# Kernel optimization log

Hardware: AMD Instinct MI355X
Metric: run time of the kernel (lower is better)

Reference implementation:

```python
import jax, jax.numpy as jnp
import numpy as np

ANNEAL_T_START = 5.0
T_END = 1.0


def setup_inputs() -> dict:
    key = jax.random.key(0)
    ks = jax.random.split(key, 8)
    B, V, H, CD, WID = 8192, 1024, 128, 16, 64
    return {
        "cond": jax.random.normal(ks[0], (B, CD), jnp.float32),
        "W": 0.01 * jax.random.normal(ks[1], (V, H), jnp.float32),
        "b": 0.01 * jax.random.normal(ks[2], (V,), jnp.float32),
        "c": 0.01 * jax.random.normal(ks[3], (H,), jnp.float32),
        "fc1_w": jax.random.normal(ks[4], (WID, CD), jnp.float32) / np.float32(np.sqrt(CD)),
        "fc1_b": jnp.zeros((WID,), jnp.float32),
        "fc2_w": jax.random.normal(ks[5], (2 * (V + H), WID), jnp.float32) / np.float32(np.sqrt(WID)),
        "fc2_b": jnp.zeros((2 * (V + H),), jnp.float32),
        "falloff": jnp.float32(1.0),
        "steps": 16,
    }


def _bern(key, p):
    # Bernoulli sample as float of same dtype as p.
    return (jax.random.uniform(key, p.shape, p.dtype) < p).astype(p.dtype)


def reference(cond, W, b, c, fc1_w, fc1_b, fc2_w, fc2_b, falloff, steps):
    V, H = W.shape
    B = cond.shape[0]
    dtype = W.dtype

    # Conditioner: FiLM-style modulation of visible/hidden biases.
    x = jnp.tanh(cond @ fc1_w.T + fc1_b)
    x = x @ fc2_w.T + fc2_b  # [B, 2*(V+H)]
    gamma_b = x[:, :V]
    beta_b = x[:, V:2 * V]
    gamma_c = x[:, 2 * V:2 * V + H]
    beta_c = x[:, 2 * V + H:]
    b_mod = (1.0 + gamma_b) * b + beta_b  # [B, V]
    c_mod = (1.0 + gamma_c) * c + beta_c  # [B, H]
    bsum = jnp.sum(b_mod, axis=-1)  # [B], constant across steps

    # Annealing temperature schedule (sigmoid falloff).
    t = jnp.arange(steps, dtype=dtype)
    s = 1.0 / (1.0 + jnp.exp(falloff * (t - steps / 2.0)))
    temps = T_END + (ANNEAL_T_START - T_END) * s  # [steps]

    base = jax.random.key(42)
    v0 = _bern(jax.random.fold_in(base, 2 ** 20), jnp.full((B, V), 0.5, dtype))
    s0_0 = jnp.ones((B, 1), dtype)

    def flip(v, s0):
        return s0 * v + (1.0 - s0) * (1.0 - v)

    def step(carry, xs):
        v, s0 = carry
        i, T = xs
        k1, k2, k3 = jax.random.split(jax.random.fold_in(base, i), 3)
        v_eff = flip(v, s0)
        p_h = jax.nn.sigmoid((v_eff @ W + c_mod) / T)  # [B, H]
        h = _bern(k1, p_h)
        a = h @ W.T  # [B, V]
        vb = jnp.sum(v * b_mod, axis=-1)
        va = jnp.sum(v * a, axis=-1)
        dE = -bsum - jnp.sum(a, axis=-1) + 2.0 * vb + 2.0 * va  # [B]
        p_s0 = jax.nn.sigmoid(dE / T)
        s0n = _bern(k2, p_s0)[:, None]  # [B, 1]
        p_v = jax.nn.sigmoid((a + b_mod) / T)
        v_samp = _bern(k3, p_v)
        v_next = flip(v_samp, s0n)
        return (v_next, s0n), None

    (v, _), _ = jax.lax.scan(
        step, (v0, s0_0), (jnp.arange(steps, dtype=jnp.int32), temps)
    )
    return v
```

## Files before the change

kernel.cpp:

```cpp
#include <hip/hip_runtime.h>
#include <stdint.h>

#pragma clang fp contract(off)

#define B_ 8192
#define V_ 1024
#define H_ 128
#define CD_ 16
#define WID_ 64
#define NOUT_ 2304
#define STEPS_ 16

typedef float f32x2 __attribute__((ext_vector_type(2)));

__device__ __forceinline__ void pkfma(f32x2& acc, f32x2 wv, f32x2 bf2) {
  asm("v_pk_fma_f32 %0, %1, %2, %0" : "+v"(acc) : "v"(wv), "v"(bf2));
}

__host__ __device__ __forceinline__ void tf2x32(uint32_t k0, uint32_t k1,
                                                uint32_t x0, uint32_t x1,
                                                uint32_t* o0, uint32_t* o1) {
  uint32_t ks2 = k0 ^ k1 ^ 0x1BD11BDAu;
#define RL_(v, d) (((v) << (d)) | ((v) >> (32 - (d))))
#define RND_(a) { x0 += x1; x1 = RL_(x1, a); x1 ^= x0; }
  x0 += k0; x1 += k1;
  RND_(13) RND_(15) RND_(26) RND_(6)
  x0 += k1; x1 += ks2 + 1u;
  RND_(17) RND_(29) RND_(16) RND_(24)
  x0 += ks2; x1 += k0 + 2u;
  RND_(13) RND_(15) RND_(26) RND_(6)
  x0 += k0; x1 += k1 + 3u;
  RND_(17) RND_(29) RND_(16) RND_(24)
  x0 += k1; x1 += ks2 + 4u;
  RND_(13) RND_(15) RND_(26) RND_(6)
  x0 += ks2; x1 += k0 + 5u;
#undef RND_
#undef RL_
  *o0 = x0; *o1 = x1;
}

struct Keys { uint32_t a[6]; };

__device__ __forceinline__ uint32_t draw_bits(uint32_t ka, uint32_t kb, uint32_t j) {
  uint32_t x0, x1;
  tf2x32(ka, kb, 0u, j, &x0, &x1);
  return x0 ^ x1;
}

__device__ __forceinline__ float bits_to_u(uint32_t bits) {
  return __fsub_rn(__uint_as_float((bits >> 9) | 0x3f800000u), 1.0f);
}

__device__ __forceinline__ float exp_a(float x) {
  float xc = fminf(fmaxf(x, -88.3762626647949f), 88.3762626647950f);
  float fx = floorf(__fadd_rn(__fmul_rn(xc, 1.44269504088896341f), 0.5f));
  float xr = __fsub_rn(xc, __fmul_rn(0.693359375f, fx));
  xr = __fsub_rn(xr, __fmul_rn(-2.12194440e-4f, fx));
  float zz = __fmul_rn(xr, xr);
  float y = 1.9875691500E-4f;
  y = __fadd_rn(__fmul_rn(y, xr), 1.3981999507E-3f);
  y = __fadd_rn(__fmul_rn(y, xr), 8.3334519073E-3f);
  y = __fadd_rn(__fmul_rn(y, xr), 4.1665795894E-2f);
  y = __fadd_rn(__fmul_rn(y, xr), 1.6666665459E-1f);
  y = __fadd_rn(__fmul_rn(y, xr), 5.0000001201E-1f);
  y = __fadd_rn(__fmul_rn(y, zz), xr);
  y = __fadd_rn(y, 1.0f);
  int n = (int)fx;
  float sc = __int_as_float((n + 127) << 23);
  return __fmul_rn(y, sc);
}

__device__ __forceinline__ float tanh_a(float xin) {
  float x = fmaxf(fminf(xin, 7.90531110763549805f), -7.90531110763549805f);
  float x2 = __fmul_rn(x, x);
  float p = __fadd_rn(__fmul_rn(x2, -2.76076847742355e-16f), 2.00018790482477e-13f);
  p = __fadd_rn(__fmul_rn(x2, p), -8.60467152213735e-11f);
  p = __fadd_rn(__fmul_rn(x2, p), 5.12229709037114e-08f);
  p = __fadd_rn(__fmul_rn(x2, p), 1.48572235717979e-05f);
  p = __fadd_rn(__fmul_rn(x2, p), 6.37261928875436e-04f);
  p = __fadd_rn(__fmul_rn(x2, p), 4.89352455891786e-03f);
  p = __fmul_rn(x, p);
  float q = __fadd_rn(__fmul_rn(x2, 1.19825839466702e-06f), 1.18534705686654e-04f);
  q = __fadd_rn(__fmul_rn(x2, q), 2.26843463243900e-03f);
  q = __fadd_rn(__fmul_rn(x2, q), 4.89352518554385e-03f);
  float r = p / q;
  if (fabsf(xin) < 0.0004f) r = xin;
  return r;
}

__device__ __forceinline__ float sigmoid_a(float z) {
  float e = exp_a(-z);
  return 1.0f / __fadd_rn(1.0f, e);
}

__global__ void k_transpose(const float* __restrict__ W, float* __restrict__ WT,
                            const float* __restrict__ fc2w, float* __restrict__ fc2T) {
  int i = blockIdx.x * blockDim.x + threadIdx.x;
  if (i < V_ * H_) { int v = i / H_, h = i % H_; WT[h * V_ + v] = W[i]; }
  if (i < NOUT_ * WID_) { int j = i / WID_, w = i % WID_; fc2T[w * NOUT_ + j] = fc2w[i]; }
}

__global__ void k_temps(const float* __restrict__ falloff, float* __restrict__ temps) {
  int t = threadIdx.x;
  if (t < 16) {
    float arg = __fmul_rn(*falloff, __fsub_rn((float)t, 8.0f));
    float e = exp_a(arg);
    float s = 1.0f / __fadd_rn(1.0f, e);
    temps[t] = __fadd_rn(1.0f, __fmul_rn(4.0f, s));
  }
}

__global__ void k_mlp1(const float* __restrict__ cond, const float* __restrict__ fc1w,
                       const float* __restrict__ fc1b, float* __restrict__ xout) {
  int idx = blockIdx.x * blockDim.x + threadIdx.x;
  if (idx >= B_ * WID_) return;
  int row = idx >> 6, w = idx & 63;
  float acc = 0.0f;
  for (int k = 0; k < CD_; k++) acc = __fmaf_rn(cond[row * CD_ + k], fc1w[w * CD_ + k], acc);
  float z = __fadd_rn(acc, fc1b[w]);
  xout[idx] = tanh_a(z);
}

__global__ __launch_bounds__(128) void k_mlp2b(const float* __restrict__ xmlp,
                       const float* __restrict__ fc2T, const float* __restrict__ fc2b,
                       const float* __restrict__ bvec, float* __restrict__ b_mod) {
  __shared__ float xs[32][WID_];
  int jbase = blockIdx.x * 128;
  int r0 = blockIdx.y * 32;
  int tid = threadIdx.x;
  for (int t = tid; t < 32 * WID_; t += 128)
    xs[t >> 6][t & 63] = xmlp[(r0 + (t >> 6)) * WID_ + (t & 63)];
  __syncthreads();
  int j = jbase + tid;
  float accg[32], accb[32];
#pragma unroll
  for (int r = 0; r < 32; r++) { accg[r] = 0.0f; accb[r] = 0.0f; }
  for (int w = 0; w < WID_; w++) {
    float fg = fc2T[w * NOUT_ + j];
    float fb = fc2T[w * NOUT_ + 1024 + j];
#pragma unroll
    for (int r = 0; r < 32; r++) {
      float xv = xs[r][w];
      accg[r] = __fmaf_rn(xv, fg, accg[r]);
      accb[r] = __fmaf_rn(xv, fb, accb[r]);
    }
  }
  float bj = bvec[j];
  float biasg = fc2b[j], biasb = fc2b[1024 + j];
#pragma unroll
  for (int r = 0; r < 32; r++) {
    float g = __fadd_rn(accg[r], biasg);
    float bb = __fadd_rn(accb[r], biasb);
    float t1 = __fadd_rn(1.0f, g);
    b_mod[(r0 + r) * V_ + j] = __fadd_rn(__fmul_rn(t1, bj), bb);
  }
}

__global__ __launch_bounds__(128) void k_mlp2c(const float* __restrict__ xmlp,
                       const float* __restrict__ fc2T, const float* __restrict__ fc2b,
                       const float* __restrict__ cvec, float* __restrict__ c_mod) {
  __shared__ float xs[32][WID_];
  int r0 = blockIdx.y * 32;
  int tid = threadIdx.x;
  for (int t = tid; t < 32 * WID_; t += 128)
    xs[t >> 6][t & 63] = xmlp[(r0 + (t >> 6)) * WID_ + (t & 63)];
  __syncthreads();
  float accg[32], accb[32];
#pragma unroll
  for (int r = 0; r < 32; r++) { accg[r] = 0.0f; accb[r] = 0.0f; }
  for (int w = 0; w < WID_; w++) {
    float fg = fc2T[w * NOUT_ + 2048 + tid];
    float fb = fc2T[w * NOUT_ + 2176 + tid];
#pragma unroll
    for (int r = 0; r < 32; r++) {
      float xv = xs[r][w];
      accg[r] = __fmaf_rn(xv, fg, accg[r]);
      accb[r] = __fmaf_rn(xv, fb, accb[r]);
    }
  }
  float cj = cvec[tid];
  float biasg = fc2b[2048 + tid], biasb = fc2b[2176 + tid];
#pragma unroll
  for (int r = 0; r < 32; r++) {
    float g = __fadd_rn(accg[r], biasg);
    float bb = __fadd_rn(accb[r], biasb);
    float t1 = __fadd_rn(1.0f, g);
    c_mod[(r0 + r) * H_ + tid] = __fadd_rn(__fmul_rn(t1, cj), bb);
  }
}

__global__ __launch_bounds__(64) void k_bsum(const float* __restrict__ b_mod,
                                             float* __restrict__ bsum) {
  int row = blockIdx.x * 64 + threadIdx.x;
  const float4* bp = (const float4*)(b_mod + (size_t)row * V_);
  float acc = 0.0f;
  for (int c = 0; c < 32; c++) {
    float4 Bv[8];
#pragma unroll
    for (int q = 0; q < 8; q++) Bv[q] = bp[c * 8 + q];
#pragma unroll
    for (int q = 0; q < 8; q++) {
      acc = __fadd_rn(acc, Bv[q].x);
      acc = __fadd_rn(acc, Bv[q].y);
      acc = __fadd_rn(acc, Bv[q].z);
      acc = __fadd_rn(acc, Bv[q].w);
    }
  }
  bsum[row] = acc;
}

__global__ void k_v0(uint32_t* __restrict__ v_bits, float* __restrict__ s0,
                     uint32_t kva, uint32_t kvb) {
  int idx = blockIdx.x * blockDim.x + threadIdx.x;
  int row = idx >> 10, col = idx & 1023;
  uint32_t bits = draw_bits(kva, kvb, (uint32_t)idx);
  float u = bits_to_u(bits);
  unsigned long long m = __ballot(u < 0.5f);
  if ((threadIdx.x & 63) == 0) {
    v_bits[row * 32 + (col >> 5)] = (uint32_t)m;
    v_bits[row * 32 + (col >> 5) + 1] = (uint32_t)(m >> 32);
  }
  if (col == 0) s0[row] = 1.0f;
}

__global__ __launch_bounds__(256) void k_h(const float* __restrict__ W,
                   const float* __restrict__ c_mod, const uint32_t* __restrict__ v_bits,
                   uint32_t* __restrict__ h_bits, const float* __restrict__ temps,
                   int step, Keys kn) {
  __shared__ uint32_t nib[16][32];
  int tid = threadIdx.x;
  int ct = tid & 31;
  int rt = tid >> 5;
  int h0 = ct << 2;
  int row0 = blockIdx.x * 16 + rt * 2;
  float T = temps[step];
  f32x2 a00 = {0.f, 0.f}, a01 = {0.f, 0.f};
  f32x2 a10 = {0.f, 0.f}, a11 = {0.f, 0.f};
  const float* wp = W + h0;
  const uint4* vb0q = (const uint4*)(v_bits + (size_t)row0 * 32);
  const uint4* vb1q = (const uint4*)(v_bits + (size_t)(row0 + 1) * 32);

  float4 A[8], Bq[8];
  uint32_t m0, m1;
  auto LOADW = [&](float4* d, int kbase) {
#pragma unroll
    for (int i = 0; i < 8; i++)
      d[i] = *(const float4*)(wp + (size_t)(kbase + i) * H_);
  };
  auto DO8 = [&](const float4* wv) {
#pragma unroll
    for (int j = 0; j < 8; j++) {
      uint32_t s0m = (uint32_t)((int32_t)m0 >> 31); m0 <<= 1;
      uint32_t s1m = (uint32_t)((int32_t)m1 >> 31); m1 <<= 1;
      float bf0 = __uint_as_float(s0m & 0x3f800000u);
      float bf1 = __uint_as_float(s1m & 0x3f800000u);
      f32x2 wlo = {wv[j].x, wv[j].y};
      f32x2 whi = {wv[j].z, wv[j].w};
      f32x2 b0 = {bf0, bf0};
      f32x2 b1 = {bf1, bf1};
      pkfma(a00, wlo, b0); pkfma(a01, whi, b0);
      pkfma(a10, wlo, b1); pkfma(a11, whi, b1);
    }
  };

  uint4 q0 = vb0q[0], q1 = vb1q[0];
  uint4 q0n, q1n;
  LOADW(A, 0);
  for (int kq = 0; kq < 8; kq++) {
    if (kq < 7) { q0n = vb0q[kq + 1]; q1n = vb1q[kq + 1]; }
    const uint32_t w0s[4] = {q0.x, q0.y, q0.z, q0.w};
    const uint32_t w1s[4] = {q1.x, q1.y, q1.z, q1.w};
#pragma unroll
    for (int wq = 0; wq < 4; wq++) {
      int kb = kq * 128 + wq * 32;
      m0 = __brev(w0s[wq]);
      m1 = __brev(w1s[wq]);
      LOADW(Bq, kb + 8);  DO8(A);
      LOADW(A, kb + 16);  DO8(Bq);
      LOADW(Bq, kb + 24); DO8(A);
      if (kb + 32 < 1024) LOADW(A, kb + 32);
      DO8(Bq);
    }
    q0 = q0n; q1 = q1n;
  }

  const f32x2* accs[2][2] = {{&a00, &a01}, {&a10, &a11}};
#pragma unroll
  for (int r = 0; r < 2; r++) {
    int row = row0 + r;
    float4 cm = *(const float4*)(c_mod + (size_t)row * H_ + h0);
    const float cma[4] = {cm.x, cm.y, cm.z, cm.w};
    const float ac[4] = {(*accs[r][0])[0], (*accs[r][0])[1],
                         (*accs[r][1])[0], (*accs[r][1])[1]};
    uint32_t nb = 0;
#pragma unroll
    for (int e = 0; e < 4; e++) {
      float z = __fadd_rn(ac[e], cma[e]) / T;
      float p = sigmoid_a(z);
      uint32_t b = draw_bits(kn.a[0], kn.a[1], (uint32_t)(row * H_ + h0 + e));
      if (bits_to_u(b) < p) nb |= 1u << e;
    }
    nib[rt * 2 + r][ct] = nb;
  }
  __syncthreads();
  if (tid < 64) {
    int rloc = tid >> 2, wq = tid & 3;
    uint32_t word = 0;
#pragma unroll
    for (int i = 0; i < 8; i++) word |= nib[rloc][wq * 8 + i] << (4 * i);
    h_bits[(size_t)(blockIdx.x * 16 + rloc) * 4 + wq] = word;
  }
}

__global__ __launch_bounds__(256) void k_a(const float* __restrict__ WT,
                   const uint32_t* __restrict__ h_bits, float* __restrict__ a) {
  int tid = threadIdx.x;
  int ct = tid & 63;
  int rt = tid >> 6;
  int v0 = blockIdx.x * 256 + (ct << 2);
  int r0 = blockIdx.y * 32 + rt * 8;
  f32x2 acc[8][2];
#pragma unroll
  for (int r = 0; r < 8; r++) { acc[r][0] = f32x2{0.f, 0.f}; acc[r][1] = f32x2{0.f, 0.f}; }
  uint4 hw[8];
#pragma unroll
  for (int r = 0; r < 8; r++) hw[r] = *(const uint4*)(h_bits + (size_t)(r0 + r) * 4);
  const float* wp0 = WT + v0;

  uint32_t m[8];
  float4 buf0[4], buf1[4];
  auto LOADG = [&](float4* d, int g) {
    const float* wp = wp0 + (size_t)(g * 4) * V_;
#pragma unroll
    for (int jj = 0; jj < 4; jj++) d[jj] = *(const float4*)(wp + (size_t)jj * V_);
  };
  auto COMP = [&](const float4* d) {
#pragma unroll
    for (int jj = 0; jj < 4; jj++) {
      f32x2 wlo = {d[jj].x, d[jj].y};
      f32x2 whi = {d[jj].z, d[jj].w};
#pragma unroll
      for (int r = 0; r < 8; r++) {
        uint32_t sm = (uint32_t)((int32_t)m[r] >> 31);
        m[r] <<= 1;
        float bf = __uint_as_float(sm & 0x3f800000u);
        f32x2 b2 = {bf, bf};
        pkfma(acc[r][0], wlo, b2);
        pkfma(acc[r][1], whi, b2);
      }
    }
  };

  LOADG(buf0, 0);
#pragma unroll
  for (int g = 0; g < 32; g++) {
    if ((g & 7) == 0) {
      const int s = g >> 3;
#pragma unroll
      for (int r = 0; r < 8; r++)
        m[r] = __brev(s == 0 ? hw[r].x : s == 1 ? hw[r].y : s == 2 ? hw[r].z : hw[r].w);
    }
    if (g & 1) { if (g < 31) LOADG(buf0, g + 1); COMP(buf1); }
    else       { if (g < 31) LOADG(buf1, g + 1); COMP(buf0); }
  }

#pragma unroll
  for (int r = 0; r < 8; r++) {
    float4 o = make_float4(acc[r][0][0], acc[r][0][1], acc[r][1][0], acc[r][1][1]);
    *(float4*)(a + (size_t)(r0 + r) * V_ + v0) = o;
  }
}

__global__ __launch_bounds__(256) void k_sv(const float* __restrict__ a,
                     const float* __restrict__ b_mod, const float* __restrict__ bsum,
                     const uint32_t* __restrict__ vb_old, uint32_t* __restrict__ vb_new,
                     float* __restrict__ s0, const float* __restrict__ temps,
                     int step, Keys kn) {
  __shared__ float As[2][16][132];
  __shared__ float Bs[2][16][132];
  int tid = threadIdx.x;
  int r0 = blockIdx.x * 16;
  float T = temps[step];
  int wv = tid >> 6;
  int lane = tid & 63;

  auto STAGE = [&](int buf, int c) {
#pragma unroll
    for (int i = 0; i < 2; i++) {
      int e = tid + i * 256;
      int r = e >> 5, c4 = e & 31;
      float4 av = *(const float4*)(a + (size_t)(r0 + r) * V_ + c * 128 + c4 * 4);
      float4 bv = *(const float4*)(b_mod + (size_t)(r0 + r) * V_ + c * 128 + c4 * 4);
      *(float4*)&As[buf][r][c4 * 4] = av;
      *(float4*)&Bs[buf][r][c4 * 4] = bv;
    }
  };

  float suma = 0.0f, vb = 0.0f, va = 0.0f;
  uint32_t flipm = 0;
  if (tid < 16) flipm = (s0[r0 + tid] == 0.0f) ? 0xFFFFFFFFu : 0u;
  STAGE(0, 0);
  __syncthreads();
  for (int c = 0; c < 8; c++) {
    if (c < 7) STAGE((c + 1) & 1, c + 1);
#pragma unroll
    for (int i = 0; i < 8; i++) {
      int e = tid + i * 256;
      int rl = e >> 7, cl = e & 127;
      float av = As[c & 1][rl][cl];
      float bv = Bs[c & 1][rl][cl];
      float z = __fadd_rn(av, bv) / T;
      float p = sigmoid_a(z);
      int row = r0 + rl;
      int col = c * 128 + cl;
      uint32_t bits = draw_bits(kn.a[4], kn.a[5], (uint32_t)(row * V_ + col));
      float u = bits_to_u(bits);
      unsigned long long mball = __ballot(u < p);
      if (lane == 0) {
        int base = row * 32 + (col >> 5);
        vb_new[base] = (uint32_t)mball;
        vb_new[base + 1] = (uint32_t)(mball >> 32);
      }
    }
    if (tid < 16) {
      int row = r0 + tid;
      uint4 mw = *(const uint4*)(vb_old + (size_t)row * 32 + c * 4);
      const uint32_t mm[4] = {mw.x ^ flipm, mw.y ^ flipm, mw.z ^ flipm, mw.w ^ flipm};
#pragma unroll
      for (int w4 = 0; w4 < 4; w4++) {
        uint32_t m = mm[w4];
#pragma unroll
        for (int j4 = 0; j4 < 8; j4++) {
          float4 av4 = *(const float4*)&As[c & 1][tid][w4 * 32 + j4 * 4];
          float4 bv4 = *(const float4*)&Bs[c & 1][tid][w4 * 32 + j4 * 4];
          const float ax[4] = {av4.x, av4.y, av4.z, av4.w};
          const float bx[4] = {bv4.x, bv4.y, bv4.z, bv4.w};
#pragma unroll
          for (int e = 0; e < 4; e++) {
            float bit = (float)((m >> (j4 * 4 + e)) & 1u);
            suma = __fadd_rn(suma, ax[e]);
            vb = __fmaf_rn(bx[e], bit, vb);
            va = __fmaf_rn(ax[e], bit, va);
          }
        }
      }
    }
    __syncthreads();
  }
  if (tid < 16) {
    int row = r0 + tid;
    float dE = __fsub_rn(-bsum[row], suma);
    dE = __fadd_rn(dE, __fmul_rn(2.0f, vb));
    dE = __fadd_rn(dE, __fmul_rn(2.0f, va));
    float p = sigmoid_a(dE / T);
    uint32_t bits = draw_bits(kn.a[2], kn.a[3], (uint32_t)row);
    float u = bits_to_u(bits);
    s0[row] = (u < p) ? 1.0f : 0.0f;
  }
}

__global__ void k_fin(const uint32_t* __restrict__ v_bits, const float* __restrict__ s0,
                      float* __restrict__ vout) {
  int idx = blockIdx.x * blockDim.x + threadIdx.x;
  int row = idx >> 10, col = idx & 1023;
  uint32_t w = v_bits[row * 32 + (col >> 5)];
  uint32_t bit = (w >> (col & 31)) & 1u;
  uint32_t eff = (s0[row] != 0.0f) ? bit : (bit ^ 1u);
  vout[idx] = (float)eff;
}

extern "C" void kernel_launch(void* const* d_in, const int* in_sizes, int n_in,
                              void* d_out, int out_size, void* d_ws, size_t ws_size,
                              hipStream_t stream) {
  const float* cond = (const float*)d_in[0];
  const float* W = (const float*)d_in[1];
  const float* bvec = (const float*)d_in[2];
  const float* cvec = (const float*)d_in[3];
  const float* fc1w = (const float*)d_in[4];
  const float* fc1b = (const float*)d_in[5];
  const float* fc2w = (const float*)d_in[6];
  const float* fc2b = (const float*)d_in[7];
  const float* falloff = (const float*)d_in[8];
  float* out = (float*)d_out;

  char* ws = (char*)d_ws;
  size_t off = 0;
  auto alloc = [&](size_t bytes) { void* p = ws + off; off += (bytes + 255) & ~(size_t)255; return p; };
  float* b_mod = (float*)alloc((size_t)B_ * V_ * 4);
  float* c_mod = (float*)alloc((size_t)B_ * H_ * 4);
  float* abuf  = (float*)alloc((size_t)B_ * V_ * 4);
  float* xmlp  = (float*)alloc((size_t)B_ * WID_ * 4);
  float* bsum  = (float*)alloc((size_t)B_ * 4);
  float* s0    = (float*)alloc((size_t)B_ * 4);
  uint32_t* v_bits0 = (uint32_t*)alloc((size_t)B_ * 32 * 4);
  uint32_t* v_bits1 = (uint32_t*)alloc((size_t)B_ * 32 * 4);
  uint32_t* h_bits = (uint32_t*)alloc((size_t)B_ * 4 * 4);
  float* WT    = (float*)alloc((size_t)H_ * V_ * 4);
  float* fc2T  = (float*)alloc((size_t)WID_ * NOUT_ * 4);
  float* temps = (float*)alloc(16 * 4);
  uint32_t* vb[2] = {v_bits0, v_bits1};

  uint32_t kva, kvb;
  tf2x32(0u, 42u, 0u, 1048576u, &kva, &kvb);
  Keys kn[16];
  for (int i = 0; i < 16; i++) {
    uint32_t f0, f1;
    tf2x32(0u, 42u, 0u, (uint32_t)i, &f0, &f1);
    uint32_t a0, a1;
    tf2x32(f0, f1, 0u, 0u, &a0, &a1); kn[i].a[0] = a0; kn[i].a[1] = a1;
    tf2x32(f0, f1, 0u, 1u, &a0, &a1); kn[i].a[2] = a0; kn[i].a[3] = a1;
    tf2x32(f0, f1, 0u, 2u, &a0, &a1); kn[i].a[4] = a0; kn[i].a[5] = a1;
  }

  k_transpose<<<(NOUT_ * WID_ + 255) / 256, 256, 0, stream>>>(W, WT, fc2w, fc2T);
  k_temps<<<1, 64, 0, stream>>>(falloff, temps);
  k_mlp1<<<(B_ * WID_) / 256, 256, 0, stream>>>(cond, fc1w, fc1b, xmlp);
  k_mlp2b<<<dim3(8, 256), 128, 0, stream>>>(xmlp, fc2T, fc2b, bvec, b_mod);
  k_mlp2c<<<dim3(1, 256), 128, 0, stream>>>(xmlp, fc2T, fc2b, cvec, c_mod);
  k_bsum<<<B_ / 64, 64, 0, stream>>>(b_mod, bsum);
  k_v0<<<(B_ * V_) / 256, 256, 0, stream>>>(vb[0], s0, kva, kvb);

  for (int i = 0; i < STEPS_; i++) {
    k_h<<<B_ / 16, 256, 0, stream>>>(W, c_mod, vb[i & 1], h_bits, temps, i, kn[i]);
    k_a<<<dim3(4, B_ / 32), 256, 0, stream>>>(WT, h_bits, abuf);
    k_sv<<<B_ / 16, 256, 0, stream>>>(abuf, b_mod, bsum, vb[i & 1], vb[(i + 1) & 1],
                                      s0, temps, i, kn[i]);
  }

  k_fin<<<(B_ * V_) / 256, 256, 0, stream>>>(vb[0], s0, out);
}
```

Before: 2.986 ms.

## Fuse visible-unit Bernoulli sampling into the h@W.T epilogue kernel

Visible sampling (sigmoid of a+b_mod, RNG draw, bit packing) moves out of the combined sample/energy kernel and into the epilogue of k_a, which packs its nibbles through shared memory into vb_new. The remaining k_s0 kernel only reduces the energy difference and samples s0. The sampling loop stays on full-block parallelism, now while the accumulators are still in registers, and k_s0 no longer does the per-element RNG work. In exchange, k_a does extra work, reads b_mod, and needs more shared memory and a block barrier.

```diff
diff --git a/kernel.cpp b/kernel.cpp
--- a/kernel.cpp
+++ b/kernel.cpp
@@ -313,7 +313,10 @@
 }
 
 __global__ __launch_bounds__(256) void k_a(const float* __restrict__ WT,
-                   const uint32_t* __restrict__ h_bits, float* __restrict__ a) {
+                   const uint32_t* __restrict__ h_bits, const float* __restrict__ b_mod,
+                   float* __restrict__ a, uint32_t* __restrict__ vb_new,
+                   const float* __restrict__ temps, int step, Keys kn) {
+  __shared__ uint32_t nib[32][65];
   int tid = threadIdx.x;
   int ct = tid & 63;
   int rt = tid >> 6;
@@ -364,25 +367,44 @@
     else       { if (g < 31) LOADG(buf1, g + 1); COMP(buf0); }
   }
 
+  float T = temps[step];
 #pragma unroll
   for (int r = 0; r < 8; r++) {
-    float4 o = make_float4(acc[r][0][0], acc[r][0][1], acc[r][1][0], acc[r][1][1]);
-    *(float4*)(a + (size_t)(r0 + r) * V_ + v0) = o;
-  }
-}
-
-__global__ __launch_bounds__(256) void k_sv(const float* __restrict__ a,
+    int row = r0 + r;
+    float4 av = make_float4(acc[r][0][0], acc[r][0][1], acc[r][1][0], acc[r][1][1]);
+    *(float4*)(a + (size_t)row * V_ + v0) = av;
+    float4 bv = *(const float4*)(b_mod + (size_t)row * V_ + v0);
+    const float ax[4] = {av.x, av.y, av.z, av.w};
+    const float bx[4] = {bv.x, bv.y, bv.z, bv.w};
+    uint32_t nb = 0;
+#pragma unroll
+    for (int e = 0; e < 4; e++) {
+      float z = __fadd_rn(ax[e], bx[e]) / T;
+      float p = sigmoid_a(z);
+      uint32_t bits = draw_bits(kn.a[4], kn.a[5], (uint32_t)(row * V_ + v0 + e));
+      float u = bits_to_u(bits);
+      if (u < p) nb |= 1u << e;
+    }
+    nib[rt * 8 + r][ct] = nb;
+  }
+  __syncthreads();
+  {
+    int rloc = tid >> 3, wq = tid & 7;
+    uint32_t word = 0;
+#pragma unroll
+    for (int i = 0; i < 8; i++) word |= nib[rloc][wq * 8 + i] << (4 * i);
+    vb_new[(size_t)(blockIdx.y * 32 + rloc) * 32 + blockIdx.x * 8 + wq] = word;
+  }
+}
+
+__global__ __launch_bounds__(256) void k_s0(const float* __restrict__ a,
                      const float* __restrict__ b_mod, const float* __restrict__ bsum,
-                     const uint32_t* __restrict__ vb_old, uint32_t* __restrict__ vb_new,
-                     float* __restrict__ s0, const float* __restrict__ temps,
-                     int step, Keys kn) {
+                     const uint32_t* __restrict__ vb_old, float* __restrict__ s0,
+                     const float* __restrict__ temps, int step, Keys kn) {
   __shared__ float As[2][16][132];
   __shared__ float Bs[2][16][132];
   int tid = threadIdx.x;
   int r0 = blockIdx.x * 16;
-  float T = temps[step];
-  int wv = tid >> 6;
-  int lane = tid & 63;
 
   auto STAGE = [&](int buf, int c) {
 #pragma unroll
@@ -403,25 +425,6 @@
   __syncthreads();
   for (int c = 0; c < 8; c++) {
     if (c < 7) STAGE((c + 1) & 1, c + 1);
-#pragma unroll
-    for (int i = 0; i < 8; i++) {
-      int e = tid + i * 256;
-      int rl = e >> 7, cl = e & 127;
-      float av = As[c & 1][rl][cl];
-      float bv = Bs[c & 1][rl][cl];
-      float z = __fadd_rn(av, bv) / T;
-      float p = sigmoid_a(z);
-      int row = r0 + rl;
-      int col = c * 128 + cl;
-      uint32_t bits = draw_bits(kn.a[4], kn.a[5], (uint32_t)(row * V_ + col));
-      float u = bits_to_u(bits);
-      unsigned long long mball = __ballot(u < p);
-      if (lane == 0) {
-        int base = row * 32 + (col >> 5);
-        vb_new[base] = (uint32_t)mball;
-        vb_new[base + 1] = (uint32_t)(mball >> 32);
-      }
-    }
     if (tid < 16) {
       int row = r0 + tid;
       uint4 mw = *(const uint4*)(vb_old + (size_t)row * 32 + c * 4);
@@ -452,6 +455,7 @@
     float dE = __fsub_rn(-bsum[row], suma);
     dE = __fadd_rn(dE, __fmul_rn(2.0f, vb));
     dE = __fadd_rn(dE, __fmul_rn(2.0f, va));
+    float T = temps[step];
     float p = sigmoid_a(dE / T);
     uint32_t bits = draw_bits(kn.a[2], kn.a[3], (uint32_t)row);
     float u = bits_to_u(bits);
@@ -522,9 +526,9 @@
 
   for (int i = 0; i < STEPS_; i++) {
     k_h<<<B_ / 16, 256, 0, stream>>>(W, c_mod, vb[i & 1], h_bits, temps, i, kn[i]);
-    k_a<<<dim3(4, B_ / 32), 256, 0, stream>>>(WT, h_bits, abuf);
-    k_sv<<<B_ / 16, 256, 0, stream>>>(abuf, b_mod, bsum, vb[i & 1], vb[(i + 1) & 1],
-                                      s0, temps, i, kn[i]);
+    k_a<<<dim3(4, B_ / 32), 256, 0, stream>>>(WT, h_bits, b_mod, abuf,
+                                              vb[(i + 1) & 1], temps, i, kn[i]);
+    k_s0<<<B_ / 16, 256, 0, stream>>>(abuf, b_mod, bsum, vb[i & 1], s0, temps, i, kn[i]);
   }
 
   k_fin<<<(B_ * V_) / 256, 256, 0, stream>>>(vb[0], s0, out);
```

After: 2.870 ms, median of 2. 3.9% less time.
